# Performance work log

Measured on AMD Instinct MI355X. Metric: run time of the kernel, lower is better.

Reference implementation:

```python
import math
import jax, jax.numpy as jnp
import numpy as np

N, B, C, H, K = 1024, 8, 512, 8, 5  # seq len, batch, d_model, heads, near_kth
NEG = -1.0e9


def setup_inputs() -> dict:
    key = jax.random.key(0)
    ks = jax.random.split(key, 10)
    s = 0.02
    return {
        "query": jax.random.normal(ks[0], (N, B, C), jnp.float32),
        "key_t": jax.random.normal(ks[1], (N, B, C), jnp.float32),
        "value": jax.random.normal(ks[2], (N, B, C), jnp.float32),
        "src_position": jax.random.normal(ks[3], (N, B, 3), jnp.float32),
        "tgt_position": jax.random.normal(ks[4], (N, B, 3), jnp.float32),
        # nn.MultiheadAttention params (in_proj split into q/k/v, plus out_proj)
        "Wq": jax.random.normal(ks[5], (C, C), jnp.float32) * s,
        "Wk": jax.random.normal(ks[6], (C, C), jnp.float32) * s,
        "Wv": jax.random.normal(ks[7], (C, C), jnp.float32) * s,
        "bq": jnp.zeros((C,), jnp.float32),
        "bk": jnp.zeros((C,), jnp.float32),
        "bv": jnp.zeros((C,), jnp.float32),
        "Wo": jax.random.normal(ks[8], (C, C), jnp.float32) * s,
        "bo": jnp.zeros((C,), jnp.float32),
    }


def reference(query, key_t, value, src_position, tgt_position,
              Wq, Wk, Wv, bq, bk, bv, Wo, bo):
    # --- 'nearby' positional mask ---------------------------------------
    # dist[b, tgt, src] = ||src_position[src,b] - tgt_position[tgt,b]||^2
    diff = src_position[None, :, :, :] - tgt_position[:, None, :, :]  # (Nt,Ns,B,3)
    dist = jnp.sum(diff * diff, axis=-1).transpose(2, 0, 1)           # (B,Nt,Ns)
    # torch: topk(dist, k=5, dim=1, largest=False) -> 5 nearest TARGETS per source
    _, idx = jax.lax.top_k(-dist.transpose(0, 2, 1), K)               # (B,Ns,K) tgt idx
    mask = jnp.full((B, N, N), NEG, jnp.float32)
    b_i = jnp.arange(B)[:, None, None]
    s_i = jnp.arange(N)[None, :, None]
    mask = mask.at[b_i, idx, s_i].set(0.0)                            # (B,Nt,Ns)

    # --- multihead attention (eval mode, dropout=0) ----------------------
    hd = C // H
    scale = 1.0 / math.sqrt(hd)
    q = ((query @ Wq.T + bq) * scale).reshape(N, B, H, hd)
    k = (key_t @ Wk.T + bk).reshape(N, B, H, hd)
    v = (value @ Wv.T + bv).reshape(N, B, H, hd)
    scores = jnp.einsum('tbhd,sbhd->bhts', q, k) + mask[:, None]      # (B,H,Nt,Ns)
    attn = jax.nn.softmax(scores, axis=-1)
    ctx = jnp.einsum('bhts,sbhd->tbhd', attn, v).reshape(N, B, C)
    out = ctx @ Wo.T + bo                                             # (N,B,C)
    attn_avg = attn.mean(axis=1)                                      # (B,Nt,Ns)
    return out, attn_avg
```

## Files before the change

### kernel.cpp

```cpp
#include <hip/hip_runtime.h>
#include <cstdint>
#include <cstddef>

#define NSEQ 1024
#define BATCH 8
#define CMODEL 512
#define NHEAD 8
#define HDIM 64
#define CAP 64
#define FLTMAX 3.402823466e+38f

typedef short bf16x8 __attribute__((ext_vector_type(8)));
typedef float f32x4 __attribute__((ext_vector_type(4)));
typedef unsigned short ushort8v __attribute__((ext_vector_type(8)));
typedef unsigned short ushort2v __attribute__((ext_vector_type(2)));

__device__ inline unsigned short f2bf(float f) {
    unsigned int u = __builtin_bit_cast(unsigned int, f);
    u += 0x7fffu + ((u >> 16) & 1u);
    return (unsigned short)(u >> 16);
}
__device__ inline float bf2f(unsigned short u) {
    return __builtin_bit_cast(float, (unsigned int)u << 16);
}

#define GLDS16(gsrc, ldst) \
    __builtin_amdgcn_global_load_lds((const __attribute__((address_space(1))) void*)(gsrc), \
                                     (__attribute__((address_space(3))) void*)(ldst), 16, 0, 0)

__global__ __launch_bounds__(256) void convert_w(const float* __restrict__ w0,
                                                 const float* __restrict__ w1,
                                                 const float* __restrict__ w2,
                                                 const float* __restrict__ w3,
                                                 unsigned short* __restrict__ o0,
                                                 unsigned short* __restrict__ o1,
                                                 unsigned short* __restrict__ o2,
                                                 unsigned short* __restrict__ o3,
                                                 unsigned int* __restrict__ zp) {
    if (blockIdx.x >= 512) {
        const int zi = (blockIdx.x - 512) * 256 + threadIdx.x;
        zp[zi] = 0u;
        return;
    }
    const int idx = blockIdx.x * 256 + threadIdx.x;
    const int rgn = idx >> 15;
    const int c   = idx & 32767;
    const float* src = rgn == 0 ? w0 : rgn == 1 ? w1 : rgn == 2 ? w2 : w3;
    unsigned short* dst = rgn == 0 ? o0 : rgn == 1 ? o1 : rgn == 2 ? o2 : o3;
    const float4 v0 = *(const float4*)(src + (size_t)c * 8);
    const float4 v1 = *(const float4*)(src + (size_t)c * 8 + 4);
    ushort8v u;
    u[0] = f2bf(v0.x); u[1] = f2bf(v0.y); u[2] = f2bf(v0.z); u[3] = f2bf(v0.w);
    u[4] = f2bf(v1.x); u[5] = f2bf(v1.y); u[6] = f2bf(v1.z); u[7] = f2bf(v1.w);
    *(ushort8v*)(dst + (size_t)c * 8) = u;
}

__global__ __launch_bounds__(256) void topk_scatter(const float* __restrict__ srcp,
                                                    const float* __restrict__ tgtp,
                                                    int* __restrict__ row_cnt,
                                                    int* __restrict__ row_list) {
    const int w = threadIdx.x >> 6, lane = threadIdx.x & 63;
    const int wg = blockIdx.x * 4 + w;
    const int s = wg & 1023, b = wg >> 10;

    const float sx = srcp[((size_t)s * BATCH + b) * 3 + 0];
    const float sy = srcp[((size_t)s * BATCH + b) * 3 + 1];
    const float sz = srcp[((size_t)s * BATCH + b) * 3 + 2];

    float dv[16];
    #pragma unroll
    for (int i = 0; i < 16; ++i) {
        const int t = i * 64 + lane;
        const float dx = tgtp[((size_t)t * BATCH + b) * 3 + 0] - sx;
        const float dy = tgtp[((size_t)t * BATCH + b) * 3 + 1] - sy;
        const float dz = tgtp[((size_t)t * BATCH + b) * 3 + 2] - sz;
        dv[i] = dx * dx + dy * dy + dz * dz;
    }

    #pragma unroll
    for (int k = 0; k < 5; ++k) {
        float bvv = FLTMAX;
        int   bii = 0x7fffffff;
        #pragma unroll
        for (int i = 0; i < 16; ++i) {
            if (dv[i] < bvv) { bvv = dv[i]; bii = i * 64 + lane; }
        }
        #pragma unroll
        for (int off = 1; off < 64; off <<= 1) {
            const float ov = __shfl_xor(bvv, off);
            const int   oi = __shfl_xor(bii, off);
            if (ov < bvv || (ov == bvv && oi < bii)) { bvv = ov; bii = oi; }
        }
        if (lane == (bii & 63)) {
            #pragma unroll
            for (int i = 0; i < 16; ++i)
                if (bii == i * 64 + lane) dv[i] = FLTMAX;
        }
        if (lane == 0) {
            const int pos = atomicAdd(&row_cnt[b * NSEQ + bii], 1);
            if (pos < CAP) row_list[((size_t)b * NSEQ + bii) * CAP + pos] = s;
        }
    }
}

template<int AMODE, int OMODE>
__device__ inline void gemm_body(const void* __restrict__ Ap,
                                 const unsigned short* __restrict__ Wbf,
                                 const float* __restrict__ bias,
                                 void* __restrict__ outp,
                                 float scale) {
    __shared__ __align__(16) char smem[24576];
    const int tid = threadIdx.x;
    const int l = tid & 63, w = tid >> 6;
    const int m0 = blockIdx.x * 128, n0 = blockIdx.y * 64;
    const int wr = (w >> 1) * 64, wc = (w & 1) * 32;
    const int lr = l & 15, g = l >> 4;

    f32x4 acc[4][2] = {};

    const int rowB = w * 16 + (l >> 2);
    const int gkB  = (l & 3) ^ ((rowB >> 1) & 3);
    const unsigned short* bsrc = Wbf + (size_t)(n0 + rowB) * CMODEL + gkB * 8;
    const int boff = 8192 + w * 1024;

    const float* asrc0 = nullptr; const float* asrc1 = nullptr;
    int adoff0 = 0, adoff1 = 0;
    const unsigned short* asrcW0 = nullptr; const unsigned short* asrcW1 = nullptr;
    int adWoff0 = 0, adWoff1 = 0;
    if constexpr (AMODE == 0) {
        const int rowA = tid >> 2;
        const int slA  = tid & 3;
        const int gkA  = slA ^ ((rowA >> 1) & 3);
        asrc0 = (const float*)Ap + (size_t)(m0 + rowA) * CMODEL + gkA * 8;
        asrc1 = asrc0 + (size_t)64 * CMODEL;
        adoff0 = rowA * 64 + slA * 16;
        adoff1 = adoff0 + 4096;
    } else {
        const unsigned short* Abf = (const unsigned short*)Ap;
        const int rA0 = w * 16 + (l >> 2);
        const int gk0 = (l & 3) ^ ((rA0 >> 1) & 3);
        asrcW0 = Abf + (size_t)(m0 + rA0) * CMODEL + gk0 * 8;
        asrcW1 = asrcW0 + (size_t)64 * CMODEL;
        adWoff0 = w * 1024;
        adWoff1 = adWoff0 + 4096;
    }

    float4 a00, a01, a10, a11;

    auto LOADA = [&](int k0) {
        a00 = *(const float4*)(asrc0 + k0); a01 = *(const float4*)(asrc0 + k0 + 4);
        a10 = *(const float4*)(asrc1 + k0); a11 = *(const float4*)(asrc1 + k0 + 4);
    };
    auto CVTSTORE = [&](int buf) {
        ushort8v u0, u1;
        u0[0] = f2bf(a00.x); u0[1] = f2bf(a00.y); u0[2] = f2bf(a00.z); u0[3] = f2bf(a00.w);
        u0[4] = f2bf(a01.x); u0[5] = f2bf(a01.y); u0[6] = f2bf(a01.z); u0[7] = f2bf(a01.w);
        u1[0] = f2bf(a10.x); u1[1] = f2bf(a10.y); u1[2] = f2bf(a10.z); u1[3] = f2bf(a10.w);
        u1[4] = f2bf(a11.x); u1[5] = f2bf(a11.y); u1[6] = f2bf(a11.z); u1[7] = f2bf(a11.w);
        char* bb = smem + buf * 12288;
        *(ushort8v*)(bb + adoff0) = u0;
        *(ushort8v*)(bb + adoff1) = u1;
    };
    auto STAGE = [&](int k0, int buf) {
        char* bb = smem + buf * 12288;
        GLDS16(bsrc + k0, bb + boff);
        if constexpr (AMODE == 1) {
            GLDS16(asrcW0 + k0, bb + adWoff0);
            GLDS16(asrcW1 + k0, bb + adWoff1);
        }
    };

    if constexpr (AMODE == 0) {
        LOADA(0);
        STAGE(0, 0);
        CVTSTORE(0);
        LOADA(32);
    } else {
        STAGE(0, 0);
    }
    __syncthreads();

    for (int t = 0; t < 16; ++t) {
        const int cur = t & 1;
        if (t < 15) {
            STAGE((t + 1) * 32, cur ^ 1);
            if constexpr (AMODE == 0) {
                CVTSTORE(cur ^ 1);
                if (t < 14) LOADA((t + 2) * 32);
            }
        }
        char* base = smem + cur * 12288;
        bf16x8 af[4], bfr[2];
        #pragma unroll
        for (int i = 0; i < 4; ++i) {
            const int ra = wr + i * 16 + lr;
            af[i] = *(const bf16x8*)(base + ra * 64 + ((g ^ ((ra >> 1) & 3)) << 4));
        }
        #pragma unroll
        for (int j = 0; j < 2; ++j) {
            const int rb = wc + j * 16 + lr;
            bfr[j] = *(const bf16x8*)(base + 8192 + rb * 64 + ((g ^ ((rb >> 1) & 3)) << 4));
        }
        #pragma unroll
        for (int i = 0; i < 4; ++i)
            #pragma unroll
            for (int j = 0; j < 2; ++j)
                acc[i][j] = __builtin_amdgcn_mfma_f32_16x16x32_bf16(af[i], bfr[j], acc[i][j], 0, 0, 0);
        __syncthreads();
    }

    #pragma unroll
    for (int i = 0; i < 4; ++i) {
        #pragma unroll
        for (int j = 0; j < 2; ++j) {
            const int col = n0 + wc + j * 16 + lr;
            const float bcol = bias[col];
            #pragma unroll
            for (int r = 0; r < 4; ++r) {
                const int row = m0 + wr + i * 16 + g * 4 + r;
                const float val = (acc[i][j][r] + bcol) * scale;
                if constexpr (OMODE == 0) {
                    const int t = row >> 3, bb = row & 7;
                    ((unsigned short*)outp)[((size_t)(bb * NSEQ + t)) * CMODEL + col] = f2bf(val);
                } else {
                    ((float*)outp)[(size_t)row * CMODEL + col] = val;
                }
            }
        }
    }
}

__global__ __launch_bounds__(256, 4) void gemm_proj(const float* __restrict__ Aq,
                                                    const float* __restrict__ Ak,
                                                    const float* __restrict__ Av,
                                                    const unsigned short* __restrict__ Wq,
                                                    const unsigned short* __restrict__ Wk,
                                                    const unsigned short* __restrict__ Wv,
                                                    const float* __restrict__ bq,
                                                    const float* __restrict__ bk,
                                                    const float* __restrict__ bv,
                                                    unsigned short* __restrict__ oq,
                                                    unsigned short* __restrict__ ok,
                                                    unsigned short* __restrict__ ov) {
    const int z = blockIdx.z;
    const float* A = z == 0 ? Aq : z == 1 ? Ak : Av;
    const unsigned short* W = z == 0 ? Wq : z == 1 ? Wk : Wv;
    const float* bi = z == 0 ? bq : z == 1 ? bk : bv;
    unsigned short* o = z == 0 ? oq : z == 1 ? ok : ov;
    const float sc = z == 0 ? 0.125f : 1.0f;
    gemm_body<0, 0>(A, W, bi, o, sc);
}

__global__ __launch_bounds__(256, 4) void gemm_out(const unsigned short* __restrict__ Abf,
                                                   const unsigned short* __restrict__ Wbf,
                                                   const float* __restrict__ bias,
                                                   float* __restrict__ out) {
    gemm_body<1, 1>(Abf, Wbf, bias, out, 1.0f);
}

__global__ __launch_bounds__(512) void v_mean_k(const unsigned short* __restrict__ v,
                                                float* __restrict__ vm) {
    const int b = blockIdx.x;
    const int chunk = blockIdx.y;
    const int c = threadIdx.x;
    float s = 0.f;
    const int t0 = chunk * 64;
    for (int t = 0; t < 64; ++t)
        s += bf2f(v[((size_t)b * NSEQ + t0 + t) * CMODEL + c]);
    atomicAdd(&vm[b * CMODEL + c], s * (1.f / (float)NSEQ));
}

__global__ __launch_bounds__(256) void sparse_attn(const unsigned short* __restrict__ q_ws,
                                                   const unsigned short* __restrict__ k_ws,
                                                   const unsigned short* __restrict__ v_ws,
                                                   const int* __restrict__ row_cnt,
                                                   const int* __restrict__ row_list,
                                                   const float* __restrict__ vm,
                                                   unsigned short* __restrict__ ctx,
                                                   float* __restrict__ attn_out) {
    const int t = blockIdx.x;
    const int b = blockIdx.y;
    const int tid = threadIdx.x;

    int cnt = row_cnt[b * NSEQ + t];
    if (cnt > CAP) cnt = CAP;

    float* arow = attn_out + ((size_t)b * NSEQ + t) * NSEQ;

    if (cnt == 0) {
        const float u = 1.f / (float)NSEQ;
        const float4 uv = {u, u, u, u};
        ((float4*)arow)[tid] = uv;
        for (int c = tid; c < CMODEL; c += 256)
            ctx[((size_t)t * BATCH + b) * CMODEL + c] = f2bf(vm[b * CMODEL + c]);
        return;
    }

    {
        const float4 zv = {0.f, 0.f, 0.f, 0.f};
        ((float4*)arow)[tid] = zv;
    }

    __shared__ float qs[CMODEL];
    __shared__ float esc[CAP][8];
    __shared__ float denom[8];
    __shared__ int   slist[CAP];

    if (tid < 8) denom[tid] = 0.f;
    if (tid < cnt) slist[tid] = row_list[((size_t)b * NSEQ + t) * CAP + tid];
    {
        const ushort2v qv = *(const ushort2v*)(q_ws + ((size_t)b * NSEQ + t) * CMODEL + tid * 2);
        qs[tid * 2] = bf2f(qv[0]); qs[tid * 2 + 1] = bf2f(qv[1]);
    }
    __syncthreads();

    const int wid = tid >> 6, lane = tid & 63;
    for (int i = wid; i < cnt; i += 4) {
        const int s = slist[i];
        const ushort8v kv = *(const ushort8v*)(k_ws + ((size_t)b * NSEQ + s) * CMODEL + lane * 8);
        const float* qrow = qs + lane * 8;
        float part = 0.f;
        #pragma unroll
        for (int j = 0; j < 8; ++j) part += qrow[j] * bf2f(kv[j]);
        part += __shfl_xor(part, 1);
        part += __shfl_xor(part, 2);
        part += __shfl_xor(part, 4);
        if ((lane & 7) == 0) {
            const int h = lane >> 3;
            const float e = __expf(part);
            esc[i][h] = e;
            atomicAdd(&denom[h], e);
        }
    }
    __syncthreads();

    for (int x = tid; x < cnt * 8; x += 256)
        esc[x >> 3][x & 7] /= denom[x & 7];
    __syncthreads();

    for (int i = tid; i < cnt; i += 256) {
        float pm = 0.f;
        #pragma unroll
        for (int h = 0; h < 8; ++h) pm += esc[i][h];
        arow[slist[i]] = pm * 0.125f;
    }

    const int c0 = tid * 2;
    const int h0 = c0 >> 6;
    float acc0 = 0.f, acc1 = 0.f;
    for (int i = 0; i < cnt; ++i) {
        const int s = slist[i];
        const float p = esc[i][h0];
        const ushort2v vv = *(const ushort2v*)(v_ws + ((size_t)b * NSEQ + s) * CMODEL + c0);
        acc0 += p * bf2f(vv[0]); acc1 += p * bf2f(vv[1]);
    }
    unsigned short* crow = ctx + ((size_t)t * BATCH + b) * CMODEL;
    ushort2v cv; cv[0] = f2bf(acc0); cv[1] = f2bf(acc1);
    *(ushort2v*)(crow + c0) = cv;
}

extern "C" void kernel_launch(void* const* d_in, const int* in_sizes, int n_in,
                              void* d_out, int out_size, void* d_ws, size_t ws_size,
                              hipStream_t stream) {
    (void)in_sizes; (void)n_in; (void)out_size; (void)ws_size;

    const float* query = (const float*)d_in[0];
    const float* key_t = (const float*)d_in[1];
    const float* value = (const float*)d_in[2];
    const float* srcp  = (const float*)d_in[3];
    const float* tgtp  = (const float*)d_in[4];
    const float* Wq    = (const float*)d_in[5];
    const float* Wk    = (const float*)d_in[6];
    const float* Wv    = (const float*)d_in[7];
    const float* bq    = (const float*)d_in[8];
    const float* bk    = (const float*)d_in[9];
    const float* bv    = (const float*)d_in[10];
    const float* Wo    = (const float*)d_in[11];
    const float* bo    = (const float*)d_in[12];

    float* out      = (float*)d_out;
    float* attn_out = out + (size_t)NSEQ * BATCH * CMODEL;

    const size_t NBC = (size_t)BATCH * NSEQ * CMODEL;
    const size_t WSZ = (size_t)CMODEL * CMODEL;
    unsigned short* q_ws  = (unsigned short*)d_ws;
    unsigned short* k_ws  = q_ws + NBC;
    unsigned short* v_ws  = k_ws + NBC;
    unsigned short* ctxbf = v_ws + NBC;
    unsigned short* wqbf  = ctxbf + NBC;
    unsigned short* wkbf  = wqbf + WSZ;
    unsigned short* wvbf  = wkbf + WSZ;
    unsigned short* wobf  = wvbf + WSZ;
    int*   row_cnt  = (int*)(wobf + WSZ);
    float* vm       = (float*)(row_cnt + BATCH * NSEQ);
    int*   row_list = (int*)(vm + BATCH * CMODEL);

    convert_w<<<560, 256, 0, stream>>>(Wq, Wk, Wv, Wo, wqbf, wkbf, wvbf, wobf,
                                       (unsigned int*)row_cnt);

    topk_scatter<<<2048, 256, 0, stream>>>(srcp, tgtp, row_cnt, row_list);

    gemm_proj<<<dim3(64, 8, 3), 256, 0, stream>>>(query, key_t, value,
                                                  wqbf, wkbf, wvbf,
                                                  bq, bk, bv,
                                                  q_ws, k_ws, v_ws);

    v_mean_k<<<dim3(BATCH, 16), 512, 0, stream>>>(v_ws, vm);

    sparse_attn<<<dim3(NSEQ, BATCH), 256, 0, stream>>>(q_ws, k_ws, v_ws, row_cnt,
                                                       row_list, vm, ctxbf, attn_out);

    gemm_out<<<dim3(64, 8), 256, 0, stream>>>(ctxbf, wobf, bo, out);
}
```

Baseline: 94.20 us.

## Pre-convert activations to bf16 and use 128x128 triple-buffered async GEMM tiles

Query, key and value activations are now converted to bf16 in a separate pass that is merged into the weight-conversion kernel. This lets both GEMMs stage A and B tiles directly to LDS with global_load_lds. The GEMM tile grows from 128x64 to 128x128 with 4x4 MFMA accumulators per wave. It uses a three-buffer pipeline with vmcnt-based waits and a raised scheduling priority around the MFMAs. The cost is an extra fp32 read and bf16 write/read round trip for the activations, plus fewer blocks per GEMM launch and lower occupancy (launch bounds 3).

```diff
diff --git a/kernel.cpp b/kernel.cpp
--- a/kernel.cpp
+++ b/kernel.cpp
@@ -28,25 +28,28 @@
     __builtin_amdgcn_global_load_lds((const __attribute__((address_space(1))) void*)(gsrc), \
                                      (__attribute__((address_space(3))) void*)(ldst), 16, 0, 0)
 
-__global__ __launch_bounds__(256) void convert_w(const float* __restrict__ w0,
-                                                 const float* __restrict__ w1,
-                                                 const float* __restrict__ w2,
-                                                 const float* __restrict__ w3,
-                                                 unsigned short* __restrict__ o0,
-                                                 unsigned short* __restrict__ o1,
-                                                 unsigned short* __restrict__ o2,
-                                                 unsigned short* __restrict__ o3,
-                                                 unsigned int* __restrict__ zp) {
-    if (blockIdx.x >= 512) {
-        const int zi = (blockIdx.x - 512) * 256 + threadIdx.x;
-        zp[zi] = 0u;
-        return;
-    }
-    const int idx = blockIdx.x * 256 + threadIdx.x;
-    const int rgn = idx >> 15;
-    const int c   = idx & 32767;
-    const float* src = rgn == 0 ? w0 : rgn == 1 ? w1 : rgn == 2 ? w2 : w3;
-    unsigned short* dst = rgn == 0 ? o0 : rgn == 1 ? o1 : rgn == 2 ? o2 : o3;
+__global__ __launch_bounds__(256) void convert_all(
+        const float* __restrict__ a0, const float* __restrict__ a1,
+        const float* __restrict__ a2,
+        const float* __restrict__ w0, const float* __restrict__ w1,
+        const float* __restrict__ w2, const float* __restrict__ w3,
+        unsigned short* __restrict__ oa0, unsigned short* __restrict__ oa1,
+        unsigned short* __restrict__ oa2,
+        unsigned short* __restrict__ ow0, unsigned short* __restrict__ ow1,
+        unsigned short* __restrict__ ow2, unsigned short* __restrict__ ow3,
+        unsigned int* __restrict__ zp) {
+    const unsigned int idx = blockIdx.x * 256 + threadIdx.x;
+    if (idx >= 1703936u) { zp[idx - 1703936u] = 0u; return; }
+    const float* src; unsigned short* dst; unsigned int c;
+    if (idx < 1572864u) {
+        const unsigned int seg = idx >> 19; c = idx & 524287u;
+        src = seg == 0 ? a0 : seg == 1 ? a1 : a2;
+        dst = seg == 0 ? oa0 : seg == 1 ? oa1 : oa2;
+    } else {
+        const unsigned int rel = idx - 1572864u, seg = rel >> 15; c = rel & 32767u;
+        src = seg == 0 ? w0 : seg == 1 ? w1 : seg == 2 ? w2 : w3;
+        dst = seg == 0 ? ow0 : seg == 1 ? ow1 : seg == 2 ? ow2 : ow3;
+    }
     const float4 v0 = *(const float4*)(src + (size_t)c * 8);
     const float4 v1 = *(const float4*)(src + (size_t)c * 8 + 4);
     ushort8v u;
@@ -103,116 +106,78 @@
     }
 }
 
-template<int AMODE, int OMODE>
-__device__ inline void gemm_body(const void* __restrict__ Ap,
+template<int OMODE>
+__device__ inline void gemm_body(const unsigned short* __restrict__ Abf,
                                  const unsigned short* __restrict__ Wbf,
                                  const float* __restrict__ bias,
-                                 void* __restrict__ outp,
-                                 float scale) {
-    __shared__ __align__(16) char smem[24576];
+                                 void* __restrict__ outp, float scale) {
+    __shared__ __align__(16) unsigned short smem[3 * 8192];
     const int tid = threadIdx.x;
     const int l = tid & 63, w = tid >> 6;
-    const int m0 = blockIdx.x * 128, n0 = blockIdx.y * 64;
-    const int wr = (w >> 1) * 64, wc = (w & 1) * 32;
+    const int m0 = blockIdx.x * 128, n0 = blockIdx.y * 128;
+    const int wr = (w >> 1) * 64, wc = (w & 1) * 64;
     const int lr = l & 15, g = l >> 4;
 
-    f32x4 acc[4][2] = {};
-
-    const int rowB = w * 16 + (l >> 2);
-    const int gkB  = (l & 3) ^ ((rowB >> 1) & 3);
-    const unsigned short* bsrc = Wbf + (size_t)(n0 + rowB) * CMODEL + gkB * 8;
-    const int boff = 8192 + w * 1024;
-
-    const float* asrc0 = nullptr; const float* asrc1 = nullptr;
-    int adoff0 = 0, adoff1 = 0;
-    const unsigned short* asrcW0 = nullptr; const unsigned short* asrcW1 = nullptr;
-    int adWoff0 = 0, adWoff1 = 0;
-    if constexpr (AMODE == 0) {
-        const int rowA = tid >> 2;
-        const int slA  = tid & 3;
-        const int gkA  = slA ^ ((rowA >> 1) & 3);
-        asrc0 = (const float*)Ap + (size_t)(m0 + rowA) * CMODEL + gkA * 8;
-        asrc1 = asrc0 + (size_t)64 * CMODEL;
-        adoff0 = rowA * 64 + slA * 16;
-        adoff1 = adoff0 + 4096;
-    } else {
-        const unsigned short* Abf = (const unsigned short*)Ap;
-        const int rA0 = w * 16 + (l >> 2);
-        const int gk0 = (l & 3) ^ ((rA0 >> 1) & 3);
-        asrcW0 = Abf + (size_t)(m0 + rA0) * CMODEL + gk0 * 8;
-        asrcW1 = asrcW0 + (size_t)64 * CMODEL;
-        adWoff0 = w * 1024;
-        adWoff1 = adWoff0 + 4096;
-    }
-
-    float4 a00, a01, a10, a11;
-
-    auto LOADA = [&](int k0) {
-        a00 = *(const float4*)(asrc0 + k0); a01 = *(const float4*)(asrc0 + k0 + 4);
-        a10 = *(const float4*)(asrc1 + k0); a11 = *(const float4*)(asrc1 + k0 + 4);
+    f32x4 acc[4][4] = {};
+
+    const int rowX = tid >> 2;
+    const int kg0  = (tid & 3) ^ ((rowX >> 1) & 3);
+    const unsigned short* aS0 = Abf + (size_t)(m0 + rowX) * CMODEL + kg0 * 8;
+    const unsigned short* aS1 = aS0 + (size_t)64 * CMODEL;
+    const unsigned short* bS0 = Wbf + (size_t)(n0 + rowX) * CMODEL + kg0 * 8;
+    const unsigned short* bS1 = bS0 + (size_t)64 * CMODEL;
+    const int wb = w * 512;
+
+    auto STAGE = [&](int k0, int buf) {
+        unsigned short* bb = smem + buf * 8192;
+        GLDS16(aS0 + k0, bb + wb);
+        GLDS16(aS1 + k0, bb + 2048 + wb);
+        GLDS16(bS0 + k0, bb + 4096 + wb);
+        GLDS16(bS1 + k0, bb + 6144 + wb);
     };
-    auto CVTSTORE = [&](int buf) {
-        ushort8v u0, u1;
-        u0[0] = f2bf(a00.x); u0[1] = f2bf(a00.y); u0[2] = f2bf(a00.z); u0[3] = f2bf(a00.w);
-        u0[4] = f2bf(a01.x); u0[5] = f2bf(a01.y); u0[6] = f2bf(a01.z); u0[7] = f2bf(a01.w);
-        u1[0] = f2bf(a10.x); u1[1] = f2bf(a10.y); u1[2] = f2bf(a10.z); u1[3] = f2bf(a10.w);
-        u1[4] = f2bf(a11.x); u1[5] = f2bf(a11.y); u1[6] = f2bf(a11.z); u1[7] = f2bf(a11.w);
-        char* bb = smem + buf * 12288;
-        *(ushort8v*)(bb + adoff0) = u0;
-        *(ushort8v*)(bb + adoff1) = u1;
-    };
-    auto STAGE = [&](int k0, int buf) {
-        char* bb = smem + buf * 12288;
-        GLDS16(bsrc + k0, bb + boff);
-        if constexpr (AMODE == 1) {
-            GLDS16(asrcW0 + k0, bb + adWoff0);
-            GLDS16(asrcW1 + k0, bb + adWoff1);
-        }
-    };
-
-    if constexpr (AMODE == 0) {
-        LOADA(0);
-        STAGE(0, 0);
-        CVTSTORE(0);
-        LOADA(32);
-    } else {
-        STAGE(0, 0);
-    }
-    __syncthreads();
-
-    for (int t = 0; t < 16; ++t) {
-        const int cur = t & 1;
-        if (t < 15) {
-            STAGE((t + 1) * 32, cur ^ 1);
-            if constexpr (AMODE == 0) {
-                CVTSTORE(cur ^ 1);
-                if (t < 14) LOADA((t + 2) * 32);
-            }
-        }
-        char* base = smem + cur * 12288;
-        bf16x8 af[4], bfr[2];
+    auto COMPUTE = [&](const unsigned short* base) {
+        bf16x8 af[4], bg[4];
         #pragma unroll
         for (int i = 0; i < 4; ++i) {
             const int ra = wr + i * 16 + lr;
-            af[i] = *(const bf16x8*)(base + ra * 64 + ((g ^ ((ra >> 1) & 3)) << 4));
-        }
-        #pragma unroll
-        for (int j = 0; j < 2; ++j) {
+            af[i] = *(const bf16x8*)(base + ra * 32 + ((g ^ ((ra >> 1) & 3)) << 3));
+        }
+        #pragma unroll
+        for (int j = 0; j < 4; ++j) {
             const int rb = wc + j * 16 + lr;
-            bfr[j] = *(const bf16x8*)(base + 8192 + rb * 64 + ((g ^ ((rb >> 1) & 3)) << 4));
-        }
+            bg[j] = *(const bf16x8*)(base + 4096 + rb * 32 + ((g ^ ((rb >> 1) & 3)) << 3));
+        }
+        __builtin_amdgcn_s_setprio(1);
         #pragma unroll
         for (int i = 0; i < 4; ++i)
             #pragma unroll
-            for (int j = 0; j < 2; ++j)
-                acc[i][j] = __builtin_amdgcn_mfma_f32_16x16x32_bf16(af[i], bfr[j], acc[i][j], 0, 0, 0);
-        __syncthreads();
-    }
+            for (int j = 0; j < 4; ++j)
+                acc[i][j] = __builtin_amdgcn_mfma_f32_16x16x32_bf16(af[i], bg[j], acc[i][j], 0, 0, 0);
+        __builtin_amdgcn_s_setprio(0);
+    };
+
+    STAGE(0, 0);
+    STAGE(32, 1);
+
+    int cur = 0;
+    for (int t = 0; t < 15; ++t) {
+        asm volatile("s_waitcnt vmcnt(4)" ::: "memory");
+        __builtin_amdgcn_s_barrier();
+        if (t < 14) {
+            int nb = cur + 2; if (nb >= 3) nb -= 3;
+            STAGE((t + 2) * 32, nb);
+        }
+        COMPUTE(smem + cur * 8192);
+        ++cur; if (cur == 3) cur = 0;
+    }
+    asm volatile("s_waitcnt vmcnt(0)" ::: "memory");
+    __builtin_amdgcn_s_barrier();
+    COMPUTE(smem + cur * 8192);
 
     #pragma unroll
     for (int i = 0; i < 4; ++i) {
         #pragma unroll
-        for (int j = 0; j < 2; ++j) {
+        for (int j = 0; j < 4; ++j) {
             const int col = n0 + wc + j * 16 + lr;
             const float bcol = bias[col];
             #pragma unroll
@@ -230,9 +195,9 @@
     }
 }
 
-__global__ __launch_bounds__(256, 4) void gemm_proj(const float* __restrict__ Aq,
-                                                    const float* __restrict__ Ak,
-                                                    const float* __restrict__ Av,
+__global__ __launch_bounds__(256, 3) void gemm_proj(const unsigned short* __restrict__ Aq,
+                                                    const unsigned short* __restrict__ Ak,
+                                                    const unsigned short* __restrict__ Av,
                                                     const unsigned short* __restrict__ Wq,
                                                     const unsigned short* __restrict__ Wk,
                                                     const unsigned short* __restrict__ Wv,
@@ -243,19 +208,19 @@
                                                     unsigned short* __restrict__ ok,
                                                     unsigned short* __restrict__ ov) {
     const int z = blockIdx.z;
-    const float* A = z == 0 ? Aq : z == 1 ? Ak : Av;
+    const unsigned short* A = z == 0 ? Aq : z == 1 ? Ak : Av;
     const unsigned short* W = z == 0 ? Wq : z == 1 ? Wk : Wv;
     const float* bi = z == 0 ? bq : z == 1 ? bk : bv;
     unsigned short* o = z == 0 ? oq : z == 1 ? ok : ov;
     const float sc = z == 0 ? 0.125f : 1.0f;
-    gemm_body<0, 0>(A, W, bi, o, sc);
-}
-
-__global__ __launch_bounds__(256, 4) void gemm_out(const unsigned short* __restrict__ Abf,
+    gemm_body<0>(A, W, bi, o, sc);
+}
+
+__global__ __launch_bounds__(256, 3) void gemm_out(const unsigned short* __restrict__ Abf,
                                                    const unsigned short* __restrict__ Wbf,
                                                    const float* __restrict__ bias,
                                                    float* __restrict__ out) {
-    gemm_body<1, 1>(Abf, Wbf, bias, out, 1.0f);
+    gemm_body<1>(Abf, Wbf, bias, out, 1.0f);
 }
 
 __global__ __launch_bounds__(512) void v_mean_k(const unsigned short* __restrict__ v,
@@ -387,7 +352,10 @@
     unsigned short* k_ws  = q_ws + NBC;
     unsigned short* v_ws  = k_ws + NBC;
     unsigned short* ctxbf = v_ws + NBC;
-    unsigned short* wqbf  = ctxbf + NBC;
+    unsigned short* qbf   = ctxbf + NBC;
+    unsigned short* kbf   = qbf + NBC;
+    unsigned short* vbf   = kbf + NBC;
+    unsigned short* wqbf  = vbf + NBC;
     unsigned short* wkbf  = wqbf + WSZ;
     unsigned short* wvbf  = wkbf + WSZ;
     unsigned short* wobf  = wvbf + WSZ;
@@ -395,12 +363,13 @@
     float* vm       = (float*)(row_cnt + BATCH * NSEQ);
     int*   row_list = (int*)(vm + BATCH * CMODEL);
 
-    convert_w<<<560, 256, 0, stream>>>(Wq, Wk, Wv, Wo, wqbf, wkbf, wvbf, wobf,
-                                       (unsigned int*)row_cnt);
+    convert_all<<<6704, 256, 0, stream>>>(query, key_t, value, Wq, Wk, Wv, Wo,
+                                          qbf, kbf, vbf, wqbf, wkbf, wvbf, wobf,
+                                          (unsigned int*)row_cnt);
 
     topk_scatter<<<2048, 256, 0, stream>>>(srcp, tgtp, row_cnt, row_list);
 
-    gemm_proj<<<dim3(64, 8, 3), 256, 0, stream>>>(query, key_t, value,
+    gemm_proj<<<dim3(64, 4, 3), 256, 0, stream>>>(qbf, kbf, vbf,
                                                   wqbf, wkbf, wvbf,
                                                   bq, bk, bv,
                                                   q_ws, k_ws, v_ws);
@@ -410,5 +379,5 @@
     sparse_attn<<<dim3(NSEQ, BATCH), 256, 0, stream>>>(q_ws, k_ws, v_ws, row_cnt,
                                                        row_list, vm, ctxbf, attn_out);
 
-    gemm_out<<<dim3(64, 8), 256, 0, stream>>>(ctxbf, wobf, bo, out);
-}
+    gemm_out<<<dim3(64, 4), 256, 0, stream>>>(ctxbf, wobf, bo, out);
+}
```

Result: faster. 90.86 us (-3.6%).
